# Optimization experiments

Measured on AMD Instinct MI355X. Metric: run time of the kernel, lower is better.

## Reference

```python
import jax, jax.numpy as jnp
import numpy as np

T, B, TACT, ACT, H = 512, 512, 48, 6, 200
IN2 = H + 48  # lstm2 / fc1 input size


def setup_inputs() -> dict:
    key = jax.random.key(0)
    ks = jax.random.split(key, 18)
    s = 0.05
    n = lambda k, shp: jax.random.normal(k, shp, dtype=jnp.float32) * s
    return {
        "tactiles": jax.random.normal(ks[0], (T, B, TACT), dtype=jnp.float32),
        "actions": jax.random.normal(ks[1], (T, B, ACT), dtype=jnp.float32),
        "fc0_w": n(ks[2], (48, 24)), "fc0_b": n(ks[3], (48,)),
        "l1_wih": n(ks[4], (4 * H, 48)), "l1_whh": n(ks[5], (4 * H, H)),
        "l1_bih": n(ks[6], (4 * H,)), "l1_bhh": n(ks[7], (4 * H,)),
        "l2_wih": n(ks[8], (4 * H, IN2)), "l2_whh": n(ks[9], (4 * H, H)),
        "l2_bih": n(ks[10], (4 * H,)), "l2_bhh": n(ks[11], (4 * H,)),
        "fc1_w": n(ks[12], (H, IN2)), "fc1_b": n(ks[13], (H,)),
        "fc2_w": n(ks[14], (48, H)), "fc2_b": n(ks[15], (48,)),
        "context_frames": 10,
    }


def _lstm_step(x, h, c, wih, whh, bih, bhh):
    # torch nn.LSTM gate order: i, f, g, o
    gates = x @ wih.T + h @ whh.T + bih + bhh  # [B, 4H]
    i, f, g, o = jnp.split(gates, 4, axis=-1)
    i, f, o = jax.nn.sigmoid(i), jax.nn.sigmoid(f), jax.nn.sigmoid(o)
    c_new = f * c + i * jnp.tanh(g)
    h_new = o * jnp.tanh(c_new)
    return h_new, c_new


def reference(tactiles, actions, fc0_w, fc0_b, l1_wih, l1_whh, l1_bih, l1_bhh,
              l2_wih, l2_whh, l2_bih, l2_bhh, fc1_w, fc1_b, fc2_w, fc2_b,
              context_frames):
    t_total, bsz = actions.shape[0], actions.shape[1]
    state = actions[0]  # [B, 6], fixed across steps

    def step(carry, inp):
        h1, c1, h2, c2, prev_out4 = carry
        tac, act, idx = inp
        # after context phase, feed back previous prediction
        x = jnp.where(idx >= context_frames, prev_out4, tac)  # [B, 48]
        h1, c1 = _lstm_step(x, h1, c1, l1_wih, l1_whh, l1_bih, l1_bhh)
        tiled = jnp.concatenate([state, state, act, act], axis=1)  # [B, 24]
        out0 = jax.nn.relu(tiled @ fc0_w.T + fc0_b)  # [B, 48]
        a_t = jnp.concatenate([h1, out0], axis=1)  # [B, 248]
        h2, c2 = _lstm_step(a_t, h2, c2, l2_wih, l2_whh, l2_bih, l2_bhh)
        lp = jnp.concatenate([h2, x], axis=1)  # [B, 248]
        out3 = jnp.tanh(lp @ fc1_w.T + fc1_b)  # [B, 200]
        out4 = jnp.tanh(out3 @ fc2_w.T + fc2_b)  # [B, 48]
        return (h1, c1, h2, c2, out4), out4

    z = jnp.zeros((bsz, H), tactiles.dtype)
    init = (z, z, z, z, jnp.zeros((bsz, 48), tactiles.dtype))
    xs = (tactiles[:-1], actions[1:], jnp.arange(t_total - 1))
    _, ys = jax.lax.scan(step, init, xs)  # [T-1, B, 48]
    # original returns [last_output(at idx cf-1)] + outputs(idx cf..T-2)
    return ys[context_frames - 1:]
```

## Files before the change

kernel.cpp:

```cpp
#include <hip/hip_runtime.h>

typedef __attribute__((ext_vector_type(8))) short short8;
typedef __attribute__((ext_vector_type(4))) float floatx4;

#define BB    512
#define HH    200
#define NSTEP 511
#define NG    32
#define NM    8
#define GWL   116

#define OW2   0
#define OW1   (OW2 + 8*112*224)
#define OF1   (OW1 + 8*112*128)
#define OF2   (OF1 + 8*32*128)
#define OFC0  (OF2 + 48*112)
#define OB1   (OFC0 + 1152)
#define OB2   (OB1 + 896)
#define OFB1  (OB2 + 896)
#define OFLG  (OFB1 + 256)
#define OEXC  (OFLG + 768)
#define WS_TOT (OEXC + NG*3*NM*400)

#define PST(p, v) __hip_atomic_store((p), (v), __ATOMIC_RELAXED, __HIP_MEMORY_SCOPE_WORKGROUP)
#define AST(p, v) __hip_atomic_store((p), (v), __ATOMIC_RELAXED, __HIP_MEMORY_SCOPE_AGENT)
#define ALD(p)    __hip_atomic_load((p), __ATOMIC_RELAXED, __HIP_MEMORY_SCOPE_AGENT)

__device__ __forceinline__ unsigned short f2bf(float f) {
    unsigned u = __float_as_uint(f);
    unsigned r = (u + 0x7fffu + ((u >> 16) & 1u)) >> 16;
    return (unsigned short)r;
}
__device__ __forceinline__ float sigm(float x) { return 1.0f / (1.0f + __expf(-x)); }
__device__ __forceinline__ float tanh_fast(float x) {
    float e = __expf(-2.0f * fabsf(x));
    float t = 1.0f - 2.0f * e / (1.0f + e);
    return copysignf(t, x);
}

__global__ void prep_kernel(const float* __restrict__ l1_wih, const float* __restrict__ l1_whh,
                            const float* __restrict__ l1_bih, const float* __restrict__ l1_bhh,
                            const float* __restrict__ l2_wih, const float* __restrict__ l2_whh,
                            const float* __restrict__ l2_bih, const float* __restrict__ l2_bhh,
                            const float* __restrict__ fc1_w, const float* __restrict__ fc2_w,
                            const float* __restrict__ fc0_w, unsigned* __restrict__ ws)
{
    int idx = blockIdx.x * blockDim.x + threadIdx.x;
    int stride = gridDim.x * blockDim.x;
    for (int i = idx; i < OEXC; i += stride) {
        if (i < OW1) {
            int r0 = i - OW2, m = r0 / (112*224), rem = r0 % (112*224);
            int r = rem / 224, kp = rem % 224;
            int grow = (r < 100) ? 200*(r/25) + 25*m + (r%25) : -1;
            float a = 0.f, b = 0.f;
            if (grow >= 0) {
                int k0 = 2*kp, k1 = k0 + 1;
                a = (k0 < 248) ? l2_wih[grow*248 + k0] : l2_whh[grow*HH + k0 - 248];
                b = (k1 < 248) ? l2_wih[grow*248 + k1] : l2_whh[grow*HH + k1 - 248];
            }
            ws[i] = (unsigned)f2bf(a) | ((unsigned)f2bf(b) << 16);
        } else if (i < OF1) {
            int r0 = i - OW1, m = r0 / (112*128), rem = r0 % (112*128);
            int r = rem / 128, kp = rem % 128;
            int grow = (r < 100) ? 200*(r/25) + 25*m + (r%25) : -1;
            float a = 0.f, b = 0.f;
            if (grow >= 0) {
                int k0 = 2*kp, k1 = k0 + 1;
                a = (k0 < 48) ? l1_wih[grow*48 + k0] : (k0 < 248 ? l1_whh[grow*HH + k0 - 48] : 0.f);
                b = (k1 < 48) ? l1_wih[grow*48 + k1] : (k1 < 248 ? l1_whh[grow*HH + k1 - 48] : 0.f);
            }
            ws[i] = (unsigned)f2bf(a) | ((unsigned)f2bf(b) << 16);
        } else if (i < OF2) {
            int r0 = i - OF1, m = r0 / (32*128), rem = r0 % (32*128);
            int r = rem / 128, kp = rem % 128;
            int frow = (r < 25) ? 25*m + r : -1;
            float a = 0.f, b = 0.f;
            if (frow >= 0) {
                int k0 = 2*kp, k1 = k0 + 1;
                a = (k0 < 248) ? fc1_w[frow*248 + k0] : 0.f;
                b = (k1 < 248) ? fc1_w[frow*248 + k1] : 0.f;
            }
            ws[i] = (unsigned)f2bf(a) | ((unsigned)f2bf(b) << 16);
        } else if (i < OFC0) {
            int r0 = i - OF2, n = r0 / 112, kp = r0 % 112;
            int k0 = 2*kp, k1 = k0 + 1;
            float a = (k0 < 200) ? fc2_w[n*HH + k0] : 0.f;
            float b = (k1 < 200) ? fc2_w[n*HH + k1] : 0.f;
            ws[i] = (unsigned)f2bf(a) | ((unsigned)f2bf(b) << 16);
        } else if (i < OB1) {
            int r = i - OFC0, k = r / 48, j = r % 48;
            ws[i] = __float_as_uint(fc0_w[j*24 + k]);
        } else if (i < OB2) {
            int r0 = i - OB1, m = r0 / 112, r = r0 % 112;
            int grow = (r < 100) ? 200*(r/25) + 25*m + (r%25) : -1;
            ws[i] = __float_as_uint(grow >= 0 ? l1_bih[grow] + l1_bhh[grow] : 0.f);
        } else if (i < OFB1) {
            int r0 = i - OB2, m = r0 / 112, r = r0 % 112;
            int grow = (r < 100) ? 200*(r/25) + 25*m + (r%25) : -1;
            ws[i] = __float_as_uint(grow >= 0 ? l2_bih[grow] + l2_bhh[grow] : 0.f);
        } else {
            ws[i] = 0u;
        }
    }
}

__global__ void prep_fc1b(const float* __restrict__ fc1_b, unsigned* __restrict__ ws)
{
    int i = blockIdx.x * blockDim.x + threadIdx.x;
    if (i < 256) {
        int m = i / 32, r = i % 32;
        ws[OFB1 + i] = __float_as_uint(r < 25 ? fc1_b[25*m + r] : 0.f);
    }
}

__device__ __forceinline__ void put16(short8* buf, int k, int m, unsigned short v) {
    int kt = k >> 5, kk = k & 31;
    ((unsigned short*)buf)[(((kt << 6) + m + ((kk >> 3) << 4)) << 3) + (kk & 7)] = v;
}

__global__ __launch_bounds__(1024, 4)
void lstm_sync(const float* __restrict__ tactiles, const float* __restrict__ actions,
               const float* __restrict__ fc0_b, const float* __restrict__ fc2_b,
               const int* __restrict__ ctxp, unsigned* __restrict__ wsu,
               float* __restrict__ out)
{
    const int tid  = threadIdx.x;
    const int lane = tid & 63, wave = tid >> 6;
    const int ln   = lane & 15, hi = lane >> 4;
    const int g    = blockIdx.x % NG;
    const int m    = blockIdx.x / NG;
    const int r0   = g * 16;
    const int ctx  = ctxp[0];

    const short8* ws8 = (const short8*)wsu;
    unsigned* flg = wsu + OFLG;
    float*    exc = (float*)(wsu + OEXC);

    __shared__ short8 sW1[112 * 33];
    __shared__ short8 sF1[32 * 33];
    __shared__ short8 sF2[48 * 29];
    __shared__ short8 XA1[8 * 64];
    __shared__ short8 XA2[14 * 64];
    __shared__ short8 XA3[8 * 64];
    __shared__ short8 XA4[7 * 64];
    __shared__ float gates[16 * GWL];
    __shared__ float b1s[112], b2s[112], f1bs[32], f2bs[48], f0bs[48];
    __shared__ float fc0s[24 * 48];
    __shared__ float st6[16][6], ac6[16][6];

    {
        const short8* w1b = ws8 + OW1/4 + m * 3584;
        for (int i = tid; i < 3584; i += 1024) sW1[(i >> 5) * 33 + (i & 31)] = w1b[i];
        const short8* f1b = ws8 + OF1/4 + m * 1024;
        for (int i = tid; i < 1024; i += 1024) sF1[(i >> 5) * 33 + (i & 31)] = f1b[i];
        const short8* f2b = ws8 + OF2/4;
        for (int i = tid; i < 1344; i += 1024) sF2[(i / 28) * 29 + (i % 28)] = f2b[i];
        short8 z = {0,0,0,0,0,0,0,0};
        for (int i = tid; i < 2368; i += 1024) {
            if (i < 512) XA1[i] = z;
            else if (i < 1408) XA2[i - 512] = z;
            else if (i < 1920) XA3[i - 1408] = z;
            else XA4[i - 1920] = z;
        }
    }
    short8 w2r[14];
    {
        short8 z = {0,0,0,0,0,0,0,0};
        #pragma unroll
        for (int kf = 0; kf < 14; ++kf) w2r[kf] = z;
        if (wave < 7) {
            const short8* w2b = ws8 + (size_t)m * 6272;
            const int rr = wave * 16 + ln;
            #pragma unroll
            for (int kf = 0; kf < 14; ++kf) w2r[kf] = w2b[rr * 56 + kf * 4 + hi];
        }
    }
    for (int i = tid; i < 112; i += 1024) {
        b1s[i] = __uint_as_float(wsu[OB1 + m*112 + i]);
        b2s[i] = __uint_as_float(wsu[OB2 + m*112 + i]);
    }
    if (tid < 32)  f1bs[tid] = __uint_as_float(wsu[OFB1 + m*32 + tid]);
    if (tid < 48)  { f2bs[tid] = fc2_b[tid]; f0bs[tid] = fc0_b[tid]; }
    for (int i = tid; i < 1152; i += 1024) fc0s[i] = __uint_as_float(wsu[OFC0 + i]);
    if (tid < 96) { int r = tid / 6, k = tid % 6; st6[r][k] = actions[(size_t)(r0 + r) * 6 + k]; }
    float c1r = 0.f, c2r = 0.f;
    __syncthreads();

    for (int t = 0; t < NSTEP; ++t) {
        if (t < ctx) {
            if (tid < 768) {
                int r = tid / 48, j = tid % 48;
                unsigned short xb = f2bf(tactiles[((size_t)t * BB + r0 + r) * 48 + j]);
                put16(XA1, j, r, xb);
                put16(XA3, 200 + j, r, xb);
            }
            __syncthreads();
        }

        if (wave < 7) {
            floatx4 acc = {0.f, 0.f, 0.f, 0.f};
            const int rbase = (wave * 16 + ln) * 33 + hi;
            #pragma unroll
            for (int kf = 0; kf < 8; ++kf)
                acc = __builtin_amdgcn_mfma_f32_16x16x32_bf16(XA1[(kf << 6) + lane], sW1[rbase + kf*4], acc, 0, 0, 0);
            int col = wave * 16 + ln, m0 = hi * 4;
            gates[(m0+0)*GWL + col] = acc[0];
            gates[(m0+1)*GWL + col] = acc[1];
            gates[(m0+2)*GWL + col] = acc[2];
            gates[(m0+3)*GWL + col] = acc[3];
        }
        if (tid >= 928) {
            int q = tid - 928, r = q / 6, k = q % 6;
            ac6[r][k] = actions[((size_t)(t + 1) * BB + r0 + r) * 6 + k];
        }
        __syncthreads();

        if (tid < 400) {
            int r = tid / 25, f = tid % 25;
            float gi = gates[r*GWL + f]      + b1s[f];
            float gf = gates[r*GWL + 25 + f] + b1s[25 + f];
            float gg = gates[r*GWL + 50 + f] + b1s[50 + f];
            float go = gates[r*GWL + 75 + f] + b1s[75 + f];
            float c = sigm(gf) * c1r + sigm(gi) * tanh_fast(gg);
            c1r = c;
            float h = sigm(go) * tanh_fast(c);
            unsigned short hb = f2bf(h);
            int kg = 25*m + f;
            put16(XA1, 48 + kg, r, hb);
            put16(XA2, kg, r, hb);
            PST(&exc[((g*3 + 0)*NM + m)*400 + tid], h);
        }
        if (tid < 768) {
            int r = tid / 48, j = tid % 48;
            float acc = f0bs[j];
            #pragma unroll
            for (int k = 0; k < 24; ++k) {
                float tv = (k < 12) ? st6[r][k % 6] : ac6[r][k % 6];
                acc += tv * fc0s[k * 48 + j];
            }
            put16(XA2, 200 + j, r, f2bf(fmaxf(acc, 0.f)));
        }
        __syncthreads();

        if (tid == 0) AST(&flg[(g*3 + 0)*NM + m], (unsigned)(t + 1));
        if (tid < 8 && tid != m) {
            while (ALD(&flg[(g*3 + 0)*NM + tid]) != (unsigned)(t + 1))
                __builtin_amdgcn_s_sleep(1);
        }
        __syncthreads();
        for (int q = tid; q < 3200; q += 1024) {
            int mm = q / 400;
            if (mm == m) continue;
            int qq = q % 400, r = qq / 25, f = qq % 25;
            float v = ALD(&exc[((g*3 + 0)*NM + mm)*400 + qq]);
            unsigned short hb = f2bf(v);
            int kg = 25*mm + f;
            put16(XA1, 48 + kg, r, hb);
            put16(XA2, kg, r, hb);
        }
        __syncthreads();

        if (wave < 7) {
            floatx4 acc = {0.f, 0.f, 0.f, 0.f};
            #pragma unroll
            for (int kf = 0; kf < 14; ++kf)
                acc = __builtin_amdgcn_mfma_f32_16x16x32_bf16(XA2[(kf << 6) + lane], w2r[kf], acc, 0, 0, 0);
            int col = wave * 16 + ln, m0 = hi * 4;
            gates[(m0+0)*GWL + col] = acc[0];
            gates[(m0+1)*GWL + col] = acc[1];
            gates[(m0+2)*GWL + col] = acc[2];
            gates[(m0+3)*GWL + col] = acc[3];
        }
        __syncthreads();

        if (tid < 400) {
            int r = tid / 25, f = tid % 25;
            float gi = gates[r*GWL + f]      + b2s[f];
            float gf = gates[r*GWL + 25 + f] + b2s[25 + f];
            float gg = gates[r*GWL + 50 + f] + b2s[50 + f];
            float go = gates[r*GWL + 75 + f] + b2s[75 + f];
            float c = sigm(gf) * c2r + sigm(gi) * tanh_fast(gg);
            c2r = c;
            float h = sigm(go) * tanh_fast(c);
            unsigned short hb = f2bf(h);
            int kg = 25*m + f;
            put16(XA2, 248 + kg, r, hb);
            put16(XA3, kg, r, hb);
            PST(&exc[((g*3 + 1)*NM + m)*400 + tid], h);
        }
        __syncthreads();

        if (tid == 0) AST(&flg[(g*3 + 1)*NM + m], (unsigned)(t + 1));
        if (tid < 8 && tid != m) {
            while (ALD(&flg[(g*3 + 1)*NM + tid]) != (unsigned)(t + 1))
                __builtin_amdgcn_s_sleep(1);
        }
        __syncthreads();
        for (int q = tid; q < 3200; q += 1024) {
            int mm = q / 400;
            if (mm == m) continue;
            int qq = q % 400, r = qq / 25, f = qq % 25;
            float v = ALD(&exc[((g*3 + 1)*NM + mm)*400 + qq]);
            unsigned short hb = f2bf(v);
            int kg = 25*mm + f;
            put16(XA2, 248 + kg, r, hb);
            put16(XA3, kg, r, hb);
        }
        __syncthreads();

        if (wave < 2) {
            floatx4 acc = {0.f, 0.f, 0.f, 0.f};
            const int rbase = (wave * 16 + ln) * 33 + hi;
            #pragma unroll
            for (int kf = 0; kf < 8; ++kf)
                acc = __builtin_amdgcn_mfma_f32_16x16x32_bf16(XA3[(kf << 6) + lane], sF1[rbase + kf*4], acc, 0, 0, 0);
            int col = wave * 16 + ln, m0 = hi * 4;
            gates[(m0+0)*GWL + col] = acc[0];
            gates[(m0+1)*GWL + col] = acc[1];
            gates[(m0+2)*GWL + col] = acc[2];
            gates[(m0+3)*GWL + col] = acc[3];
        }
        __syncthreads();

        if (tid < 400) {
            int r = tid / 25, f = tid % 25;
            float v = tanh_fast(gates[r*GWL + f] + f1bs[f]);
            put16(XA4, 25*m + f, r, f2bf(v));
            PST(&exc[((g*3 + 2)*NM + m)*400 + tid], v);
        }
        __syncthreads();

        if (tid == 0) AST(&flg[(g*3 + 2)*NM + m], (unsigned)(t + 1));
        if (tid < 8 && tid != m) {
            while (ALD(&flg[(g*3 + 2)*NM + tid]) != (unsigned)(t + 1))
                __builtin_amdgcn_s_sleep(1);
        }
        __syncthreads();
        for (int q = tid; q < 3200; q += 1024) {
            int mm = q / 400;
            if (mm == m) continue;
            int qq = q % 400, r = qq / 25, f = qq % 25;
            float v = ALD(&exc[((g*3 + 2)*NM + mm)*400 + qq]);
            put16(XA4, 25*mm + f, r, f2bf(v));
        }
        __syncthreads();

        if (wave < 3) {
            floatx4 acc = {0.f, 0.f, 0.f, 0.f};
            const int rbase = (wave * 16 + ln) * 29 + hi;
            #pragma unroll
            for (int kf = 0; kf < 7; ++kf)
                acc = __builtin_amdgcn_mfma_f32_16x16x32_bf16(XA4[(kf << 6) + lane], sF2[rbase + kf*4], acc, 0, 0, 0);
            int col = wave * 16 + ln, m0 = hi * 4;
            gates[(m0+0)*GWL + col] = acc[0];
            gates[(m0+1)*GWL + col] = acc[1];
            gates[(m0+2)*GWL + col] = acc[2];
            gates[(m0+3)*GWL + col] = acc[3];
        }
        __syncthreads();

        if (tid < 768) {
            int r = tid / 48, j = tid % 48;
            float v = tanh_fast(gates[r*GWL + j] + f2bs[j]);
            unsigned short xb = f2bf(v);
            put16(XA1, j, r, xb);
            put16(XA3, 200 + j, r, xb);
            if (m == 0 && t >= ctx - 1)
                out[((size_t)(t - (ctx - 1)) * BB + r0 + r) * 48 + j] = v;
        }
        __syncthreads();
    }
}

extern "C" void kernel_launch(void* const* d_in, const int* in_sizes, int n_in,
                              void* d_out, int out_size, void* d_ws, size_t ws_size,
                              hipStream_t stream)
{
    const float* tactiles = (const float*)d_in[0];
    const float* actions  = (const float*)d_in[1];
    const float* fc0_w    = (const float*)d_in[2];
    const float* fc0_b    = (const float*)d_in[3];
    const float* l1_wih   = (const float*)d_in[4];
    const float* l1_whh   = (const float*)d_in[5];
    const float* l1_bih   = (const float*)d_in[6];
    const float* l1_bhh   = (const float*)d_in[7];
    const float* l2_wih   = (const float*)d_in[8];
    const float* l2_whh   = (const float*)d_in[9];
    const float* l2_bih   = (const float*)d_in[10];
    const float* l2_bhh   = (const float*)d_in[11];
    const float* fc1_w    = (const float*)d_in[12];
    const float* fc1_b    = (const float*)d_in[13];
    const float* fc2_w    = (const float*)d_in[14];
    const float* fc2_b    = (const float*)d_in[15];
    const int*   ctxp     = (const int*)d_in[16];
    unsigned* ws = (unsigned*)d_ws;
    float* out = (float*)d_out;

    hipLaunchKernelGGL(prep_kernel, dim3(512), dim3(256), 0, stream,
                       l1_wih, l1_whh, l1_bih, l1_bhh,
                       l2_wih, l2_whh, l2_bih, l2_bhh,
                       fc1_w, fc2_w, fc0_w, ws);
    hipLaunchKernelGGL(prep_fc1b, dim3(1), dim3(256), 0, stream, fc1_b, ws);
    hipLaunchKernelGGL(lstm_sync, dim3(256), dim3(1024), 0, stream,
                       tactiles, actions, fc0_b, fc2_b, ctxp, ws, out);
}
```

Baseline: 3.674 ms.

## Unify activation buffers into one shared layout and fold biases into GEMMs

Merges the four separate bf16 activation staging buffers into a single combined K-layout (x, h1, bias-one column, fc0 output, h2), so each hidden state is written once instead of twice. Biases are folded into the weight matrices through a constant-one column, which removes the per-step bias adds. fc2 weights move into registers of otherwise idle waves, the separate fc1 bias prep kernel is dropped, and the cross-block flag wait becomes a wave-wide ballot poll without a block barrier. The cost is wider K for the layer-2 and fc1 MFMAs (more MFMA work per step, fc1 doubles to 16 k-steps) and a bf16-rounded bias.

New measurement: 3.952 ms. 1.08x slower.

```diff
diff --git a/kernel.cpp b/kernel.cpp
--- a/kernel.cpp
+++ b/kernel.cpp
@@ -4,21 +4,17 @@
 typedef __attribute__((ext_vector_type(4))) float floatx4;
 
 #define BB    512
-#define HH    200
 #define NSTEP 511
 #define NG    32
 #define NM    8
 #define GWL   116
 
 #define OW2   0
-#define OW1   (OW2 + 8*112*224)
+#define OW1   (OW2 + 8*112*240)
 #define OF1   (OW1 + 8*112*128)
-#define OF2   (OF1 + 8*32*128)
+#define OF2   (OF1 + 8*32*256)
 #define OFC0  (OF2 + 48*112)
-#define OB1   (OFC0 + 1152)
-#define OB2   (OB1 + 896)
-#define OFB1  (OB2 + 896)
-#define OFLG  (OFB1 + 256)
+#define OFLG  (OFC0 + 1152)
 #define OEXC  (OFLG + 768)
 #define WS_TOT (OEXC + NG*3*NM*400)
 
@@ -38,78 +34,85 @@
     return copysignf(t, x);
 }
 
+__device__ __forceinline__ float w1val(int k, int grow,
+        const float* l1_wih, const float* l1_whh, const float* l1_bih, const float* l1_bhh) {
+    if (k < 48)  return l1_wih[grow*48 + k];
+    if (k < 248) return l1_whh[grow*200 + (k - 48)];
+    if (k == 248) return l1_bih[grow] + l1_bhh[grow];
+    return 0.f;
+}
+__device__ __forceinline__ float w2val(int k, int grow,
+        const float* l2_wih, const float* l2_whh, const float* l2_bih, const float* l2_bhh) {
+    if (k >= 48 && k < 248) return l2_wih[grow*248 + (k - 48)];
+    if (k == 248) return l2_bih[grow] + l2_bhh[grow];
+    if (k >= 256 && k < 304) return l2_wih[grow*248 + 200 + (k - 256)];
+    if (k >= 304 && k < 504) return l2_whh[grow*200 + (k - 304)];
+    return 0.f;
+}
+__device__ __forceinline__ float f1val(int k, int frow,
+        const float* fc1_w, const float* fc1_b) {
+    if (k < 48) return fc1_w[frow*248 + 200 + k];
+    if (k == 248) return fc1_b[frow];
+    if (k >= 304 && k < 504) return fc1_w[frow*248 + (k - 304)];
+    return 0.f;
+}
+
 __global__ void prep_kernel(const float* __restrict__ l1_wih, const float* __restrict__ l1_whh,
                             const float* __restrict__ l1_bih, const float* __restrict__ l1_bhh,
                             const float* __restrict__ l2_wih, const float* __restrict__ l2_whh,
                             const float* __restrict__ l2_bih, const float* __restrict__ l2_bhh,
-                            const float* __restrict__ fc1_w, const float* __restrict__ fc2_w,
+                            const float* __restrict__ fc1_w, const float* __restrict__ fc1_b,
+                            const float* __restrict__ fc2_w, const float* __restrict__ fc2_b,
                             const float* __restrict__ fc0_w, unsigned* __restrict__ ws)
 {
     int idx = blockIdx.x * blockDim.x + threadIdx.x;
     int stride = gridDim.x * blockDim.x;
     for (int i = idx; i < OEXC; i += stride) {
         if (i < OW1) {
-            int r0 = i - OW2, m = r0 / (112*224), rem = r0 % (112*224);
-            int r = rem / 224, kp = rem % 224;
+            int r0 = i - OW2, m = r0 / 26880, rem = r0 % 26880;
+            int r = rem / 240, kp = rem % 240;
+            int k0 = 32 + 2*kp, k1 = k0 + 1;
             int grow = (r < 100) ? 200*(r/25) + 25*m + (r%25) : -1;
             float a = 0.f, b = 0.f;
             if (grow >= 0) {
-                int k0 = 2*kp, k1 = k0 + 1;
-                a = (k0 < 248) ? l2_wih[grow*248 + k0] : l2_whh[grow*HH + k0 - 248];
-                b = (k1 < 248) ? l2_wih[grow*248 + k1] : l2_whh[grow*HH + k1 - 248];
+                a = w2val(k0, grow, l2_wih, l2_whh, l2_bih, l2_bhh);
+                b = w2val(k1, grow, l2_wih, l2_whh, l2_bih, l2_bhh);
             }
             ws[i] = (unsigned)f2bf(a) | ((unsigned)f2bf(b) << 16);
         } else if (i < OF1) {
-            int r0 = i - OW1, m = r0 / (112*128), rem = r0 % (112*128);
+            int r0 = i - OW1, m = r0 / 14336, rem = r0 % 14336;
             int r = rem / 128, kp = rem % 128;
+            int k0 = 2*kp, k1 = k0 + 1;
             int grow = (r < 100) ? 200*(r/25) + 25*m + (r%25) : -1;
             float a = 0.f, b = 0.f;
             if (grow >= 0) {
-                int k0 = 2*kp, k1 = k0 + 1;
-                a = (k0 < 48) ? l1_wih[grow*48 + k0] : (k0 < 248 ? l1_whh[grow*HH + k0 - 48] : 0.f);
-                b = (k1 < 48) ? l1_wih[grow*48 + k1] : (k1 < 248 ? l1_whh[grow*HH + k1 - 48] : 0.f);
+                a = w1val(k0, grow, l1_wih, l1_whh, l1_bih, l1_bhh);
+                b = w1val(k1, grow, l1_wih, l1_whh, l1_bih, l1_bhh);
             }
             ws[i] = (unsigned)f2bf(a) | ((unsigned)f2bf(b) << 16);
         } else if (i < OF2) {
-            int r0 = i - OF1, m = r0 / (32*128), rem = r0 % (32*128);
-            int r = rem / 128, kp = rem % 128;
-            int frow = (r < 25) ? 25*m + r : -1;
+            int r0 = i - OF1, m = r0 / 8192, rem = r0 % 8192;
+            int r = rem / 256, kp = rem % 256;
+            int k0 = 2*kp, k1 = k0 + 1;
             float a = 0.f, b = 0.f;
-            if (frow >= 0) {
-                int k0 = 2*kp, k1 = k0 + 1;
-                a = (k0 < 248) ? fc1_w[frow*248 + k0] : 0.f;
-                b = (k1 < 248) ? fc1_w[frow*248 + k1] : 0.f;
+            if (r < 25) {
+                int frow = 25*m + r;
+                a = f1val(k0, frow, fc1_w, fc1_b);
+                b = f1val(k1, frow, fc1_w, fc1_b);
             }
             ws[i] = (unsigned)f2bf(a) | ((unsigned)f2bf(b) << 16);
         } else if (i < OFC0) {
             int r0 = i - OF2, n = r0 / 112, kp = r0 % 112;
             int k0 = 2*kp, k1 = k0 + 1;
-            float a = (k0 < 200) ? fc2_w[n*HH + k0] : 0.f;
-            float b = (k1 < 200) ? fc2_w[n*HH + k1] : 0.f;
+            float a = (k0 < 200) ? fc2_w[n*200 + k0] : (k0 == 200 ? fc2_b[n] : 0.f);
+            float b = (k1 < 200) ? fc2_w[n*200 + k1] : (k1 == 200 ? fc2_b[n] : 0.f);
             ws[i] = (unsigned)f2bf(a) | ((unsigned)f2bf(b) << 16);
-        } else if (i < OB1) {
+        } else if (i < OFLG) {
             int r = i - OFC0, k = r / 48, j = r % 48;
             ws[i] = __float_as_uint(fc0_w[j*24 + k]);
-        } else if (i < OB2) {
-            int r0 = i - OB1, m = r0 / 112, r = r0 % 112;
-            int grow = (r < 100) ? 200*(r/25) + 25*m + (r%25) : -1;
-            ws[i] = __float_as_uint(grow >= 0 ? l1_bih[grow] + l1_bhh[grow] : 0.f);
-        } else if (i < OFB1) {
-            int r0 = i - OB2, m = r0 / 112, r = r0 % 112;
-            int grow = (r < 100) ? 200*(r/25) + 25*m + (r%25) : -1;
-            ws[i] = __float_as_uint(grow >= 0 ? l2_bih[grow] + l2_bhh[grow] : 0.f);
         } else {
             ws[i] = 0u;
         }
-    }
-}
-
-__global__ void prep_fc1b(const float* __restrict__ fc1_b, unsigned* __restrict__ ws)
-{
-    int i = blockIdx.x * blockDim.x + threadIdx.x;
-    if (i < 256) {
-        int m = i / 32, r = i % 32;
-        ws[OFB1 + i] = __float_as_uint(r < 25 ? fc1_b[25*m + r] : 0.f);
     }
 }
 
@@ -120,9 +123,8 @@
 
 __global__ __launch_bounds__(1024, 4)
 void lstm_sync(const float* __restrict__ tactiles, const float* __restrict__ actions,
-               const float* __restrict__ fc0_b, const float* __restrict__ fc2_b,
-               const int* __restrict__ ctxp, unsigned* __restrict__ wsu,
-               float* __restrict__ out)
+               const float* __restrict__ fc0_b, const int* __restrict__ ctxp,
+               unsigned* __restrict__ wsu, float* __restrict__ out)
 {
     const int tid  = threadIdx.x;
     const int lane = tid & 63, wave = tid >> 6;
@@ -137,52 +139,50 @@
     float*    exc = (float*)(wsu + OEXC);
 
     __shared__ short8 sW1[112 * 33];
-    __shared__ short8 sF1[32 * 33];
-    __shared__ short8 sF2[48 * 29];
-    __shared__ short8 XA1[8 * 64];
-    __shared__ short8 XA2[14 * 64];
-    __shared__ short8 XA3[8 * 64];
+    __shared__ short8 sF1[32 * 65];
+    __shared__ short8 XAC[16 * 64];
     __shared__ short8 XA4[7 * 64];
     __shared__ float gates[16 * GWL];
-    __shared__ float b1s[112], b2s[112], f1bs[32], f2bs[48], f0bs[48];
+    __shared__ float f0bs[48];
     __shared__ float fc0s[24 * 48];
     __shared__ float st6[16][6], ac6[16][6];
 
     {
         const short8* w1b = ws8 + OW1/4 + m * 3584;
         for (int i = tid; i < 3584; i += 1024) sW1[(i >> 5) * 33 + (i & 31)] = w1b[i];
-        const short8* f1b = ws8 + OF1/4 + m * 1024;
-        for (int i = tid; i < 1024; i += 1024) sF1[(i >> 5) * 33 + (i & 31)] = f1b[i];
-        const short8* f2b = ws8 + OF2/4;
-        for (int i = tid; i < 1344; i += 1024) sF2[(i / 28) * 29 + (i % 28)] = f2b[i];
+        const short8* f1b = ws8 + OF1/4 + m * 2048;
+        for (int i = tid; i < 2048; i += 1024) sF1[(i >> 6) * 65 + (i & 63)] = f1b[i];
         short8 z = {0,0,0,0,0,0,0,0};
-        for (int i = tid; i < 2368; i += 1024) {
-            if (i < 512) XA1[i] = z;
-            else if (i < 1408) XA2[i - 512] = z;
-            else if (i < 1920) XA3[i - 1408] = z;
-            else XA4[i - 1920] = z;
+        for (int i = tid; i < 1024 + 448; i += 1024) {
+            if (i < 1024) XAC[i] = z;
+            else XA4[i - 1024] = z;
         }
     }
-    short8 w2r[14];
+    short8 wreg[15];
     {
         short8 z = {0,0,0,0,0,0,0,0};
         #pragma unroll
-        for (int kf = 0; kf < 14; ++kf) w2r[kf] = z;
+        for (int kf = 0; kf < 15; ++kf) wreg[kf] = z;
         if (wave < 7) {
-            const short8* w2b = ws8 + (size_t)m * 6272;
+            const short8* w2b = ws8 + OW2/4 + (size_t)m * 6720;
             const int rr = wave * 16 + ln;
             #pragma unroll
-            for (int kf = 0; kf < 14; ++kf) w2r[kf] = w2b[rr * 56 + kf * 4 + hi];
+            for (int kf = 0; kf < 15; ++kf) wreg[kf] = w2b[rr * 60 + kf * 4 + hi];
+        } else if (wave >= 8 && wave < 11) {
+            const short8* f2b = ws8 + OF2/4;
+            const int rr = (wave - 8) * 16 + ln;
+            #pragma unroll
+            for (int kf = 0; kf < 7; ++kf) wreg[kf] = f2b[rr * 28 + kf * 4 + hi];
         }
     }
-    for (int i = tid; i < 112; i += 1024) {
-        b1s[i] = __uint_as_float(wsu[OB1 + m*112 + i]);
-        b2s[i] = __uint_as_float(wsu[OB2 + m*112 + i]);
-    }
-    if (tid < 32)  f1bs[tid] = __uint_as_float(wsu[OFB1 + m*32 + tid]);
-    if (tid < 48)  { f2bs[tid] = fc2_b[tid]; f0bs[tid] = fc0_b[tid]; }
+    if (tid < 48) f0bs[tid] = fc0_b[tid];
     for (int i = tid; i < 1152; i += 1024) fc0s[i] = __uint_as_float(wsu[OFC0 + i]);
     if (tid < 96) { int r = tid / 6, k = tid % 6; st6[r][k] = actions[(size_t)(r0 + r) * 6 + k]; }
+    __syncthreads();
+    if (tid < 16) {
+        put16(XAC, 248, tid, (unsigned short)0x3F80);
+        put16(XA4, 200, tid, (unsigned short)0x3F80);
+    }
     float c1r = 0.f, c2r = 0.f;
     __syncthreads();
 
@@ -190,9 +190,7 @@
         if (t < ctx) {
             if (tid < 768) {
                 int r = tid / 48, j = tid % 48;
-                unsigned short xb = f2bf(tactiles[((size_t)t * BB + r0 + r) * 48 + j]);
-                put16(XA1, j, r, xb);
-                put16(XA3, 200 + j, r, xb);
+                put16(XAC, j, r, f2bf(tactiles[((size_t)t * BB + r0 + r) * 48 + j]));
             }
             __syncthreads();
         }
@@ -202,7 +200,7 @@
             const int rbase = (wave * 16 + ln) * 33 + hi;
             #pragma unroll
             for (int kf = 0; kf < 8; ++kf)
-                acc = __builtin_amdgcn_mfma_f32_16x16x32_bf16(XA1[(kf << 6) + lane], sW1[rbase + kf*4], acc, 0, 0, 0);
+                acc = __builtin_amdgcn_mfma_f32_16x16x32_bf16(XAC[(kf << 6) + lane], sW1[rbase + kf*4], acc, 0, 0, 0);
             int col = wave * 16 + ln, m0 = hi * 4;
             gates[(m0+0)*GWL + col] = acc[0];
             gates[(m0+1)*GWL + col] = acc[1];
@@ -217,54 +215,56 @@
 
         if (tid < 400) {
             int r = tid / 25, f = tid % 25;
-            float gi = gates[r*GWL + f]      + b1s[f];
-            float gf = gates[r*GWL + 25 + f] + b1s[25 + f];
-            float gg = gates[r*GWL + 50 + f] + b1s[50 + f];
-            float go = gates[r*GWL + 75 + f] + b1s[75 + f];
+            float gi = gates[r*GWL + f];
+            float gf = gates[r*GWL + 25 + f];
+            float gg = gates[r*GWL + 50 + f];
+            float go = gates[r*GWL + 75 + f];
             float c = sigm(gf) * c1r + sigm(gi) * tanh_fast(gg);
             c1r = c;
             float h = sigm(go) * tanh_fast(c);
-            unsigned short hb = f2bf(h);
-            int kg = 25*m + f;
-            put16(XA1, 48 + kg, r, hb);
-            put16(XA2, kg, r, hb);
+            put16(XAC, 48 + 25*m + f, r, f2bf(h));
             PST(&exc[((g*3 + 0)*NM + m)*400 + tid], h);
-        }
-        if (tid < 768) {
-            int r = tid / 48, j = tid % 48;
-            float acc = f0bs[j];
-            #pragma unroll
-            for (int k = 0; k < 24; ++k) {
-                float tv = (k < 12) ? st6[r][k % 6] : ac6[r][k % 6];
-                acc += tv * fc0s[k * 48 + j];
-            }
-            put16(XA2, 200 + j, r, f2bf(fmaxf(acc, 0.f)));
+        } else {
+            int q = tid - 400;
+            #pragma unroll
+            for (int rep = 0; rep < 2; ++rep) {
+                int item = q + rep * 624;
+                if (item < 768) {
+                    int r = item / 48, j = item % 48;
+                    float acc = f0bs[j];
+                    #pragma unroll
+                    for (int k = 0; k < 24; ++k) {
+                        float tv = (k < 12) ? st6[r][k % 6] : ac6[r][k % 6];
+                        acc += tv * fc0s[k * 48 + j];
+                    }
+                    put16(XAC, 256 + j, r, f2bf(fmaxf(acc, 0.f)));
+                }
+            }
         }
         __syncthreads();
 
         if (tid == 0) AST(&flg[(g*3 + 0)*NM + m], (unsigned)(t + 1));
-        if (tid < 8 && tid != m) {
-            while (ALD(&flg[(g*3 + 0)*NM + tid]) != (unsigned)(t + 1))
+        {
+            unsigned got = (lane < NM) ? ALD(&flg[(g*3 + 0)*NM + lane]) : (unsigned)(t + 1);
+            while (__ballot(got != (unsigned)(t + 1)) != 0ULL) {
                 __builtin_amdgcn_s_sleep(1);
-        }
-        __syncthreads();
+                if (lane < NM) got = ALD(&flg[(g*3 + 0)*NM + lane]);
+            }
+        }
         for (int q = tid; q < 3200; q += 1024) {
             int mm = q / 400;
             if (mm == m) continue;
             int qq = q % 400, r = qq / 25, f = qq % 25;
             float v = ALD(&exc[((g*3 + 0)*NM + mm)*400 + qq]);
-            unsigned short hb = f2bf(v);
-            int kg = 25*mm + f;
-            put16(XA1, 48 + kg, r, hb);
-            put16(XA2, kg, r, hb);
+            put16(XAC, 48 + 25*mm + f, r, f2bf(v));
         }
         __syncthreads();
 
         if (wave < 7) {
             floatx4 acc = {0.f, 0.f, 0.f, 0.f};
             #pragma unroll
-            for (int kf = 0; kf < 14; ++kf)
-                acc = __builtin_amdgcn_mfma_f32_16x16x32_bf16(XA2[(kf << 6) + lane], w2r[kf], acc, 0, 0, 0);
+            for (int kf = 0; kf < 15; ++kf)
+                acc = __builtin_amdgcn_mfma_f32_16x16x32_bf16(XAC[((kf + 1) << 6) + lane], wreg[kf], acc, 0, 0, 0);
             int col = wave * 16 + ln, m0 = hi * 4;
             gates[(m0+0)*GWL + col] = acc[0];
             gates[(m0+1)*GWL + col] = acc[1];
@@ -275,45 +275,41 @@
 
         if (tid < 400) {
             int r = tid / 25, f = tid % 25;
-            float gi = gates[r*GWL + f]      + b2s[f];
-            float gf = gates[r*GWL + 25 + f] + b2s[25 + f];
-            float gg = gates[r*GWL + 50 + f] + b2s[50 + f];
-            float go = gates[r*GWL + 75 + f] + b2s[75 + f];
+            float gi = gates[r*GWL + f];
+            float gf = gates[r*GWL + 25 + f];
+            float gg = gates[r*GWL + 50 + f];
+            float go = gates[r*GWL + 75 + f];
             float c = sigm(gf) * c2r + sigm(gi) * tanh_fast(gg);
             c2r = c;
             float h = sigm(go) * tanh_fast(c);
-            unsigned short hb = f2bf(h);
-            int kg = 25*m + f;
-            put16(XA2, 248 + kg, r, hb);
-            put16(XA3, kg, r, hb);
+            put16(XAC, 304 + 25*m + f, r, f2bf(h));
             PST(&exc[((g*3 + 1)*NM + m)*400 + tid], h);
         }
         __syncthreads();
 
         if (tid == 0) AST(&flg[(g*3 + 1)*NM + m], (unsigned)(t + 1));
-        if (tid < 8 && tid != m) {
-            while (ALD(&flg[(g*3 + 1)*NM + tid]) != (unsigned)(t + 1))
+        {
+            unsigned got = (lane < NM) ? ALD(&flg[(g*3 + 1)*NM + lane]) : (unsigned)(t + 1);
+            while (__ballot(got != (unsigned)(t + 1)) != 0ULL) {
                 __builtin_amdgcn_s_sleep(1);
-        }
-        __syncthreads();
+                if (lane < NM) got = ALD(&flg[(g*3 + 1)*NM + lane]);
+            }
+        }
         for (int q = tid; q < 3200; q += 1024) {
             int mm = q / 400;
             if (mm == m) continue;
             int qq = q % 400, r = qq / 25, f = qq % 25;
             float v = ALD(&exc[((g*3 + 1)*NM + mm)*400 + qq]);
-            unsigned short hb = f2bf(v);
-            int kg = 25*mm + f;
-            put16(XA2, 248 + kg, r, hb);
-            put16(XA3, kg, r, hb);
+            put16(XAC, 304 + 25*mm + f, r, f2bf(v));
         }
         __syncthreads();
 
         if (wave < 2) {
             floatx4 acc = {0.f, 0.f, 0.f, 0.f};
-            const int rbase = (wave * 16 + ln) * 33 + hi;
-            #pragma unroll
-            for (int kf = 0; kf < 8; ++kf)
-                acc = __builtin_amdgcn_mfma_f32_16x16x32_bf16(XA3[(kf << 6) + lane], sF1[rbase + kf*4], acc, 0, 0, 0);
+            const int rbase = (wave * 16 + ln) * 65 + hi;
+            #pragma unroll
+            for (int kf = 0; kf < 16; ++kf)
+                acc = __builtin_amdgcn_mfma_f32_16x16x32_bf16(XAC[(kf << 6) + lane], sF1[rbase + kf*4], acc, 0, 0, 0);
             int col = wave * 16 + ln, m0 = hi * 4;
             gates[(m0+0)*GWL + col] = acc[0];
             gates[(m0+1)*GWL + col] = acc[1];
@@ -324,18 +320,20 @@
 
         if (tid < 400) {
             int r = tid / 25, f = tid % 25;
-            float v = tanh_fast(gates[r*GWL + f] + f1bs[f]);
+            float v = tanh_fast(gates[r*GWL + f]);
             put16(XA4, 25*m + f, r, f2bf(v));
             PST(&exc[((g*3 + 2)*NM + m)*400 + tid], v);
         }
         __syncthreads();
 
         if (tid == 0) AST(&flg[(g*3 + 2)*NM + m], (unsigned)(t + 1));
-        if (tid < 8 && tid != m) {
-            while (ALD(&flg[(g*3 + 2)*NM + tid]) != (unsigned)(t + 1))
+        {
+            unsigned got = (lane < NM) ? ALD(&flg[(g*3 + 2)*NM + lane]) : (unsigned)(t + 1);
+            while (__ballot(got != (unsigned)(t + 1)) != 0ULL) {
                 __builtin_amdgcn_s_sleep(1);
-        }
-        __syncthreads();
+                if (lane < NM) got = ALD(&flg[(g*3 + 2)*NM + lane]);
+            }
+        }
         for (int q = tid; q < 3200; q += 1024) {
             int mm = q / 400;
             if (mm == m) continue;
@@ -345,13 +343,12 @@
         }
         __syncthreads();
 
-        if (wave < 3) {
+        if (wave >= 8 && wave < 11) {
             floatx4 acc = {0.f, 0.f, 0.f, 0.f};
-            const int rbase = (wave * 16 + ln) * 29 + hi;
             #pragma unroll
             for (int kf = 0; kf < 7; ++kf)
-                acc = __builtin_amdgcn_mfma_f32_16x16x32_bf16(XA4[(kf << 6) + lane], sF2[rbase + kf*4], acc, 0, 0, 0);
-            int col = wave * 16 + ln, m0 = hi * 4;
+                acc = __builtin_amdgcn_mfma_f32_16x16x32_bf16(XA4[(kf << 6) + lane], wreg[kf], acc, 0, 0, 0);
+            int col = (wave - 8) * 16 + ln, m0 = hi * 4;
             gates[(m0+0)*GWL + col] = acc[0];
             gates[(m0+1)*GWL + col] = acc[1];
             gates[(m0+2)*GWL + col] = acc[2];
@@ -361,10 +358,8 @@
 
         if (tid < 768) {
             int r = tid / 48, j = tid % 48;
-            float v = tanh_fast(gates[r*GWL + j] + f2bs[j]);
-            unsigned short xb = f2bf(v);
-            put16(XA1, j, r, xb);
-            put16(XA3, 200 + j, r, xb);
+            float v = tanh_fast(gates[r*GWL + j]);
+            if (t + 1 >= ctx) put16(XAC, j, r, f2bf(v));
             if (m == 0 && t >= ctx - 1)
                 out[((size_t)(t - (ctx - 1)) * BB + r0 + r) * 48 + j] = v;
         }
@@ -399,8 +394,7 @@
     hipLaunchKernelGGL(prep_kernel, dim3(512), dim3(256), 0, stream,
                        l1_wih, l1_whh, l1_bih, l1_bhh,
                        l2_wih, l2_whh, l2_bih, l2_bhh,
-                       fc1_w, fc2_w, fc0_w, ws);
-    hipLaunchKernelGGL(prep_fc1b, dim3(1), dim3(256), 0, stream, fc1_b, ws);
+                       fc1_w, fc1_b, fc2_w, fc2_b, fc0_w, ws);
     hipLaunchKernelGGL(lstm_sync, dim3(256), dim3(1024), 0, stream,
-                       tactiles, actions, fc0_b, fc2_b, ctxp, ws, out);
-}
+                       tactiles, actions, fc0_b, ctxp, ws, out);
+}
```
